# Performance work log

Hardware: AMD Instinct MI355X
Metric: run time of the kernel (lower is better)

The kernel has to match this reference:

```python
import jax, jax.numpy as jnp
import numpy as np
import math


def _rope_2d(k, height, width):
    """Additive 2D sinusoidal position embedding. k: (B, N, D), N == height*width."""
    B, N, D = k.shape
    d_half = D // 2
    y_idx = jnp.arange(height, dtype=jnp.float32) / max(height - 1, 1)
    x_idx = jnp.arange(width, dtype=jnp.float32) / max(width - 1, 1)
    y_grid, x_grid = jnp.meshgrid(y_idx, x_idx, indexing='ij')
    y_flat = y_grid.reshape(-1)  # (N,)
    x_flat = x_grid.reshape(-1)
    freq = jnp.exp(jnp.arange(0, d_half, 2, dtype=jnp.float32) * (-(math.log(10000.0) / d_half)))

    def pos_half(flat, scale):
        ang = flat[:, None] * freq[None, :] * scale  # (N, ceil(d_half/2))
        p = jnp.zeros((N, d_half), dtype=jnp.float32)
        p = p.at[:, 0::2].set(jnp.sin(ang))
        n_odd = p[:, 1::2].shape[-1]
        p = p.at[:, 1::2].set(jnp.cos(ang[:, :n_odd]))
        return p

    pos_emb = jnp.concatenate([pos_half(y_flat, float(height)), pos_half(x_flat, float(width))], axis=-1)
    if pos_emb.shape[-1] < D:
        pos_emb = jnp.pad(pos_emb, ((0, 0), (0, D - pos_emb.shape[-1])))
    elif pos_emb.shape[-1] > D:
        pos_emb = pos_emb[:, :D]
    return k + pos_emb[None]


def setup_inputs() -> dict:
    key = jax.random.key(0)
    k1, k2, k3, k4 = jax.random.split(key, 4)
    B, N, dim = 2, 4096, 768
    num_heads, key_dim = 2, 8
    # xavier-uniform-like scales
    sq = math.sqrt(6.0 / (dim + num_heads * (key_dim + 1)))
    sk = math.sqrt(6.0 / (dim + key_dim))
    return {
        'query_tokens': jax.random.normal(k1, (B, N, dim), dtype=jnp.float32),
        'key_tokens': jax.random.normal(k2, (B, N, dim), dtype=jnp.float32),
        'Wq': jax.random.uniform(k3, (dim, num_heads * (key_dim + 1)), minval=-sq, maxval=sq, dtype=jnp.float32),
        'Wk': jax.random.uniform(k4, (dim, key_dim), minval=-sk, maxval=sk, dtype=jnp.float32),
        'spatial_bias': jnp.zeros((1, 1, 1), dtype=jnp.float32),
        'height': 64,
        'width': 64,
    }


def reference(query_tokens, key_tokens, Wq, Wk, spatial_bias, height, width):
    key_dim = Wk.shape[-1]
    num_heads = Wq.shape[-1] // (key_dim + 1)
    scale = key_dim ** (-0.5)
    B, N_q, _ = query_tokens.shape
    qw = (query_tokens @ Wq).reshape(B, N_q, num_heads, key_dim + 1)
    q = qw[..., :key_dim]          # (B, Nq, H, d)
    w = qw[..., -1]                # (B, Nq, H)
    k = key_tokens @ Wk            # (B, Nk, d)
    if height is not None and width is not None:
        k = _rope_2d(k, height, width)
    scores = jax.nn.relu(jnp.einsum('bqhd,bkd->bhqk', q, k) * scale)  # (B,H,Nq,Nk)
    index_scores = jnp.einsum('bqh,bhqk->bqk', w, scores)
    return index_scores + spatial_bias
```

## Files before the change

kernel.cpp:

```cpp
#include <hip/hip_runtime.h>
#include <math.h>

#define BB 2
#define NN 4096
#define DIM 768
#define QSTRIDE 20
#define KT 128

typedef float f32x4 __attribute__((ext_vector_type(4)));

__global__ __launch_bounds__(256) void proj_kernel(const float* __restrict__ xq,
                                                   const float* __restrict__ Wq,
                                                   float* __restrict__ qd,
                                                   const float* __restrict__ xk,
                                                   const float* __restrict__ Wk,
                                                   const int* __restrict__ hp,
                                                   const int* __restrict__ wp,
                                                   float* __restrict__ kd) {
  const int lane = threadIdx.x & 63;
  const int pair = blockIdx.x * 4 + (threadIdx.x >> 6);
  const int row0 = pair * 2;

  if (blockIdx.y == 0) {
    const float* xr0 = xq + (size_t)row0 * DIM;
    const float* xr1 = xr0 + DIM;

    float acc0[18], acc1[18];
#pragma unroll
    for (int c = 0; c < 18; ++c) { acc0[c] = 0.f; acc1[c] = 0.f; }

#pragma unroll
    for (int j = 0; j < DIM / 64; ++j) {
      const int i = lane + 64 * j;
      const float x0 = xr0[i];
      const float x1 = xr1[i];
      const float* wr = Wq + i * 18;
#pragma unroll
      for (int c = 0; c < 9; ++c) {
        const float2 w2 = *(const float2*)(wr + 2 * c);
        acc0[2 * c]     = fmaf(x0, w2.x, acc0[2 * c]);
        acc0[2 * c + 1] = fmaf(x0, w2.y, acc0[2 * c + 1]);
        acc1[2 * c]     = fmaf(x1, w2.x, acc1[2 * c]);
        acc1[2 * c + 1] = fmaf(x1, w2.y, acc1[2 * c + 1]);
      }
    }

#pragma unroll
    for (int off = 32; off >= 1; off >>= 1) {
#pragma unroll
      for (int c = 0; c < 18; ++c) {
        acc0[c] += __shfl_xor(acc0[c], off, 64);
        acc1[c] += __shfl_xor(acc1[c], off, 64);
      }
    }

    const int r = lane >> 5;
    const int l = lane & 31;
    if (l < 18) {
      int src;
      if (l < 8) src = l;
      else if (l < 16) src = l + 1;
      else if (l == 16) src = 8;
      else src = 17;
      float v = r ? acc1[0] : acc0[0];
#pragma unroll
      for (int c = 1; c < 18; ++c) {
        const float cand = r ? acc1[c] : acc0[c];
        v = (src == c) ? cand : v;
      }
      qd[(size_t)(row0 + r) * QSTRIDE + l] = v;
    }
  } else {
    const float* xr0 = xk + (size_t)row0 * DIM;
    const float* xr1 = xr0 + DIM;

    float acc0[8], acc1[8];
#pragma unroll
    for (int c = 0; c < 8; ++c) { acc0[c] = 0.f; acc1[c] = 0.f; }

#pragma unroll
    for (int j = 0; j < DIM / 64; ++j) {
      const int i = lane + 64 * j;
      const float x0 = xr0[i];
      const float x1 = xr1[i];
      const float4 wa = *(const float4*)(Wk + i * 8);
      const float4 wb = *(const float4*)(Wk + i * 8 + 4);
      acc0[0] = fmaf(x0, wa.x, acc0[0]); acc0[1] = fmaf(x0, wa.y, acc0[1]);
      acc0[2] = fmaf(x0, wa.z, acc0[2]); acc0[3] = fmaf(x0, wa.w, acc0[3]);
      acc0[4] = fmaf(x0, wb.x, acc0[4]); acc0[5] = fmaf(x0, wb.y, acc0[5]);
      acc0[6] = fmaf(x0, wb.z, acc0[6]); acc0[7] = fmaf(x0, wb.w, acc0[7]);
      acc1[0] = fmaf(x1, wa.x, acc1[0]); acc1[1] = fmaf(x1, wa.y, acc1[1]);
      acc1[2] = fmaf(x1, wa.z, acc1[2]); acc1[3] = fmaf(x1, wa.w, acc1[3]);
      acc1[4] = fmaf(x1, wb.x, acc1[4]); acc1[5] = fmaf(x1, wb.y, acc1[5]);
      acc1[6] = fmaf(x1, wb.z, acc1[6]); acc1[7] = fmaf(x1, wb.w, acc1[7]);
    }

#pragma unroll
    for (int off = 32; off >= 1; off >>= 1) {
#pragma unroll
      for (int c = 0; c < 8; ++c) {
        acc0[c] += __shfl_xor(acc0[c], off, 64);
        acc1[c] += __shfl_xor(acc1[c], off, 64);
      }
    }

    const int r = lane >> 5;
    const int l = lane & 31;
    if (l < 8) {
      const int row = row0 + r;
      const int h = hp[0];
      const int w = wp[0];
      const int n = row % NN;
      const int yi = n / w;
      const int xi = n - yi * w;
      const int hd = (h - 1) > 1 ? (h - 1) : 1;
      const int wd = (w - 1) > 1 ? (w - 1) : 1;
      const float yv = (float)yi / (float)hd;
      const float xv = (float)xi / (float)wd;
      const float base = (l < 4) ? yv : xv;
      const float sc = (l < 4) ? (float)h : (float)w;
      const float fr = (l & 2) ? 0.01f : 1.0f;
      const float ang = base * fr * sc;
      const float pe = (l & 1) ? cosf(ang) : sinf(ang);
      float v = r ? acc1[0] : acc0[0];
#pragma unroll
      for (int c = 1; c < 8; ++c) {
        const float cand = r ? acc1[c] : acc0[c];
        v = (l == c) ? cand : v;
      }
      kd[(size_t)row * 8 + l] = v + pe;
    }
  }
}

__device__ __forceinline__ float dot8(const float4 a, const float4 b,
                                      const float* __restrict__ k8) {
  float d = a.x * k8[0];
  d = fmaf(a.y, k8[1], d);
  d = fmaf(a.z, k8[2], d);
  d = fmaf(a.w, k8[3], d);
  d = fmaf(b.x, k8[4], d);
  d = fmaf(b.y, k8[5], d);
  d = fmaf(b.z, k8[6], d);
  d = fmaf(b.w, k8[7], d);
  return d;
}

__global__ __launch_bounds__(256) void scores_kernel(const float* __restrict__ qd,
                                                     const float* __restrict__ kd,
                                                     const float* __restrict__ bias,
                                                     float* __restrict__ out) {
  __shared__ float ks[KT * 9];
  __shared__ float qs[32 * QSTRIDE];

  const int tid = threadIdx.x;
  const int kb = blockIdx.x;
  const int qb = blockIdx.y;
  const int b  = blockIdx.z;

  {
    const float4 v = ((const float4*)(kd + ((size_t)b * NN + kb * KT) * 8))[tid];
    const int key = tid >> 1;
    const int off = (tid & 1) * 4;
    float* dst = ks + key * 9 + off;
    dst[0] = v.x; dst[1] = v.y; dst[2] = v.z; dst[3] = v.w;
  }
  if (tid < 160) {
    ((float4*)qs)[tid] = ((const float4*)(qd + ((size_t)b * NN + qb * 32) * QSTRIDE))[tid];
  }
  __syncthreads();

  const int tx = tid & 15;
  const int ty = tid >> 4;
  const float sb = bias[0];
  const float scale = 0.35355339059327373f;

  const int k0 = tx * 8;
  float kv[8][8];
#pragma unroll
  for (int i = 0; i < 8; ++i) {
    const float* kp = ks + (k0 + i) * 9;
#pragma unroll
    for (int d = 0; d < 8; ++d) kv[i][d] = kp[d];
  }

#pragma unroll
  for (int qi = 0; qi < 2; ++qi) {
    const int lq = ty * 2 + qi;
    const float* qp = qs + lq * QSTRIDE;
    const float4 a0 = *(const float4*)(qp);
    const float4 a1 = *(const float4*)(qp + 4);
    const float4 b0 = *(const float4*)(qp + 8);
    const float4 b1 = *(const float4*)(qp + 12);
    const float w0 = qp[16];
    const float w1 = qp[17];

    f32x4 res[2];
    float* r = (float*)res;
#pragma unroll
    for (int i = 0; i < 8; ++i) {
      float d0 = dot8(a0, a1, kv[i]);
      float d1 = dot8(b0, b1, kv[i]);
      d0 = fmaxf(d0 * scale, 0.f);
      d1 = fmaxf(d1 * scale, 0.f);
      r[i] = fmaf(w0, d0, fmaf(w1, d1, sb));
    }

    const int q = qb * 32 + lq;
    float* op = out + ((size_t)b * NN + q) * (size_t)NN + (size_t)(kb * KT + k0);
    __builtin_nontemporal_store(res[0], (f32x4*)op);
    __builtin_nontemporal_store(res[1], (f32x4*)(op + 4));
  }
}

extern "C" void kernel_launch(void* const* d_in, const int* in_sizes, int n_in,
                              void* d_out, int out_size, void* d_ws, size_t ws_size,
                              hipStream_t stream) {
  const float* qt = (const float*)d_in[0];
  const float* kt = (const float*)d_in[1];
  const float* Wq = (const float*)d_in[2];
  const float* Wk = (const float*)d_in[3];
  const float* sb = (const float*)d_in[4];
  const int* hp = (const int*)d_in[5];
  const int* wp = (const int*)d_in[6];

  float* qd = (float*)d_ws;
  float* kd = qd + (size_t)BB * NN * QSTRIDE;
  float* outp = (float*)d_out;

  proj_kernel<<<dim3(BB * NN / 8, 2), 256, 0, stream>>>(qt, Wq, qd, kt, Wk, hp, wp, kd);
  scores_kernel<<<dim3(NN / KT, NN / 32, BB), 256, 0, stream>>>(qd, kd, sb, outp);
}
```

Before: 210.7 us.

## Vectorize projection input loads and switch score stores to strided scalar writes

The projection kernel now loads activations as float4 per lane, with each lane covering four consecutive elements, instead of one scalar per lane. In the scores kernel each thread now handles keys strided by 16 rather than 8 contiguous keys. Outputs are written as plain scalar stores with a 16-element stride, replacing 16-byte nontemporal vector stores. The intent is likely fewer load instructions and lane-coalesced output writes, but it gives up vector and nontemporal stores on the dominant 128MB output write. The strided key reads from LDS also change the bank access pattern.

Measured after the change: 212.4 us. About the same (+0.8%).

```diff
diff --git a/kernel.cpp b/kernel.cpp
--- a/kernel.cpp
+++ b/kernel.cpp
@@ -6,8 +6,6 @@
 #define DIM 768
 #define QSTRIDE 20
 #define KT 128
-
-typedef float f32x4 __attribute__((ext_vector_type(4)));
 
 __global__ __launch_bounds__(256) void proj_kernel(const float* __restrict__ xq,
                                                    const float* __restrict__ Wq,
@@ -30,18 +28,23 @@
     for (int c = 0; c < 18; ++c) { acc0[c] = 0.f; acc1[c] = 0.f; }
 
 #pragma unroll
-    for (int j = 0; j < DIM / 64; ++j) {
-      const int i = lane + 64 * j;
-      const float x0 = xr0[i];
-      const float x1 = xr1[i];
-      const float* wr = Wq + i * 18;
-#pragma unroll
-      for (int c = 0; c < 9; ++c) {
-        const float2 w2 = *(const float2*)(wr + 2 * c);
-        acc0[2 * c]     = fmaf(x0, w2.x, acc0[2 * c]);
-        acc0[2 * c + 1] = fmaf(x0, w2.y, acc0[2 * c + 1]);
-        acc1[2 * c]     = fmaf(x1, w2.x, acc1[2 * c]);
-        acc1[2 * c + 1] = fmaf(x1, w2.y, acc1[2 * c + 1]);
+    for (int j = 0; j < DIM / 256; ++j) {
+      const int i0 = 4 * lane + 256 * j;
+      const float4 x0v = *(const float4*)(xr0 + i0);
+      const float4 x1v = *(const float4*)(xr1 + i0);
+#pragma unroll
+      for (int e = 0; e < 4; ++e) {
+        const float x0 = ((const float*)&x0v)[e];
+        const float x1 = ((const float*)&x1v)[e];
+        const float* wr = Wq + (size_t)(i0 + e) * 18;
+#pragma unroll
+        for (int c = 0; c < 9; ++c) {
+          const float2 w2 = *(const float2*)(wr + 2 * c);
+          acc0[2 * c]     = fmaf(x0, w2.x, acc0[2 * c]);
+          acc0[2 * c + 1] = fmaf(x0, w2.y, acc0[2 * c + 1]);
+          acc1[2 * c]     = fmaf(x1, w2.x, acc1[2 * c]);
+          acc1[2 * c + 1] = fmaf(x1, w2.y, acc1[2 * c + 1]);
+        }
       }
     }
 
@@ -79,20 +82,25 @@
     for (int c = 0; c < 8; ++c) { acc0[c] = 0.f; acc1[c] = 0.f; }
 
 #pragma unroll
-    for (int j = 0; j < DIM / 64; ++j) {
-      const int i = lane + 64 * j;
-      const float x0 = xr0[i];
-      const float x1 = xr1[i];
-      const float4 wa = *(const float4*)(Wk + i * 8);
-      const float4 wb = *(const float4*)(Wk + i * 8 + 4);
-      acc0[0] = fmaf(x0, wa.x, acc0[0]); acc0[1] = fmaf(x0, wa.y, acc0[1]);
-      acc0[2] = fmaf(x0, wa.z, acc0[2]); acc0[3] = fmaf(x0, wa.w, acc0[3]);
-      acc0[4] = fmaf(x0, wb.x, acc0[4]); acc0[5] = fmaf(x0, wb.y, acc0[5]);
-      acc0[6] = fmaf(x0, wb.z, acc0[6]); acc0[7] = fmaf(x0, wb.w, acc0[7]);
-      acc1[0] = fmaf(x1, wa.x, acc1[0]); acc1[1] = fmaf(x1, wa.y, acc1[1]);
-      acc1[2] = fmaf(x1, wa.z, acc1[2]); acc1[3] = fmaf(x1, wa.w, acc1[3]);
-      acc1[4] = fmaf(x1, wb.x, acc1[4]); acc1[5] = fmaf(x1, wb.y, acc1[5]);
-      acc1[6] = fmaf(x1, wb.z, acc1[6]); acc1[7] = fmaf(x1, wb.w, acc1[7]);
+    for (int j = 0; j < DIM / 256; ++j) {
+      const int i0 = 4 * lane + 256 * j;
+      const float4 x0v = *(const float4*)(xr0 + i0);
+      const float4 x1v = *(const float4*)(xr1 + i0);
+#pragma unroll
+      for (int e = 0; e < 4; ++e) {
+        const float x0 = ((const float*)&x0v)[e];
+        const float x1 = ((const float*)&x1v)[e];
+        const float4 wa = *(const float4*)(Wk + (size_t)(i0 + e) * 8);
+        const float4 wb = *(const float4*)(Wk + (size_t)(i0 + e) * 8 + 4);
+        acc0[0] = fmaf(x0, wa.x, acc0[0]); acc0[1] = fmaf(x0, wa.y, acc0[1]);
+        acc0[2] = fmaf(x0, wa.z, acc0[2]); acc0[3] = fmaf(x0, wa.w, acc0[3]);
+        acc0[4] = fmaf(x0, wb.x, acc0[4]); acc0[5] = fmaf(x0, wb.y, acc0[5]);
+        acc0[6] = fmaf(x0, wb.z, acc0[6]); acc0[7] = fmaf(x0, wb.w, acc0[7]);
+        acc1[0] = fmaf(x1, wa.x, acc1[0]); acc1[1] = fmaf(x1, wa.y, acc1[1]);
+        acc1[2] = fmaf(x1, wa.z, acc1[2]); acc1[3] = fmaf(x1, wa.w, acc1[3]);
+        acc1[4] = fmaf(x1, wb.x, acc1[4]); acc1[5] = fmaf(x1, wb.y, acc1[5]);
+        acc1[6] = fmaf(x1, wb.z, acc1[6]); acc1[7] = fmaf(x1, wb.w, acc1[7]);
+      }
     }
 
 #pragma unroll
@@ -133,19 +141,6 @@
   }
 }
 
-__device__ __forceinline__ float dot8(const float4 a, const float4 b,
-                                      const float* __restrict__ k8) {
-  float d = a.x * k8[0];
-  d = fmaf(a.y, k8[1], d);
-  d = fmaf(a.z, k8[2], d);
-  d = fmaf(a.w, k8[3], d);
-  d = fmaf(b.x, k8[4], d);
-  d = fmaf(b.y, k8[5], d);
-  d = fmaf(b.z, k8[6], d);
-  d = fmaf(b.w, k8[7], d);
-  return d;
-}
-
 __global__ __launch_bounds__(256) void scores_kernel(const float* __restrict__ qd,
                                                      const float* __restrict__ kd,
                                                      const float* __restrict__ bias,
@@ -175,11 +170,10 @@
   const float sb = bias[0];
   const float scale = 0.35355339059327373f;
 
-  const int k0 = tx * 8;
   float kv[8][8];
 #pragma unroll
   for (int i = 0; i < 8; ++i) {
-    const float* kp = ks + (k0 + i) * 9;
+    const float* kp = ks + (tx + 16 * i) * 9;
 #pragma unroll
     for (int d = 0; d < 8; ++d) kv[i][d] = kp[d];
   }
@@ -195,21 +189,27 @@
     const float w0 = qp[16];
     const float w1 = qp[17];
 
-    f32x4 res[2];
-    float* r = (float*)res;
+    float r[8];
 #pragma unroll
     for (int i = 0; i < 8; ++i) {
-      float d0 = dot8(a0, a1, kv[i]);
-      float d1 = dot8(b0, b1, kv[i]);
+      float d0 = kv[i][0] * a0.x;
+      float d1 = kv[i][0] * b0.x;
+      d0 = fmaf(a0.y, kv[i][1], d0); d1 = fmaf(b0.y, kv[i][1], d1);
+      d0 = fmaf(a0.z, kv[i][2], d0); d1 = fmaf(b0.z, kv[i][2], d1);
+      d0 = fmaf(a0.w, kv[i][3], d0); d1 = fmaf(b0.w, kv[i][3], d1);
+      d0 = fmaf(a1.x, kv[i][4], d0); d1 = fmaf(b1.x, kv[i][4], d1);
+      d0 = fmaf(a1.y, kv[i][5], d0); d1 = fmaf(b1.y, kv[i][5], d1);
+      d0 = fmaf(a1.z, kv[i][6], d0); d1 = fmaf(b1.z, kv[i][6], d1);
+      d0 = fmaf(a1.w, kv[i][7], d0); d1 = fmaf(b1.w, kv[i][7], d1);
       d0 = fmaxf(d0 * scale, 0.f);
       d1 = fmaxf(d1 * scale, 0.f);
       r[i] = fmaf(w0, d0, fmaf(w1, d1, sb));
     }
 
     const int q = qb * 32 + lq;
-    float* op = out + ((size_t)b * NN + q) * (size_t)NN + (size_t)(kb * KT + k0);
-    __builtin_nontemporal_store(res[0], (f32x4*)op);
-    __builtin_nontemporal_store(res[1], (f32x4*)(op + 4));
+    float* op = out + ((size_t)b * NN + q) * (size_t)NN + (size_t)(kb * KT + tx);
+#pragma unroll
+    for (int i = 0; i < 8; ++i) op[16 * i] = r[i];
   }
 }
 
```
